# Kernel optimization log

Hardware: AMD Instinct MI355X
Metric: run time of the kernel (lower is better)

The kernel has to match this reference:

```python
import jax, jax.numpy as jnp
import numpy as np

EPS = 1e-8  # torch F.cosine_similarity eps


def setup_inputs() -> dict:
    key = jax.random.key(0)
    k1, k2, k3, k4 = jax.random.split(key, 4)
    B, N, D = 16384, 4096, 1024
    return {
        "query": jax.random.normal(k1, (B, D), dtype=jnp.float32),
        "prompt_components": 0.02 * jax.random.normal(k2, (N, D), dtype=jnp.float32),
        "component_keys": 0.02 * jax.random.normal(k3, (N, D), dtype=jnp.float32),
        "component_attention": 0.02 * jax.random.normal(k4, (N, D), dtype=jnp.float32),
        "top_k": 8,
    }


def reference(query, prompt_components, component_keys, component_attention, top_k):
    # attended query: elementwise scale by mean attention vector
    attn_mean = component_attention.mean(axis=0)            # [D]
    aq = query * attn_mean                                   # [B, D]

    # cosine similarity vs detached keys (vectorized over all components)
    keys = jax.lax.stop_gradient(component_keys)             # detach, as in torch
    aq_n = aq / jnp.maximum(jnp.linalg.norm(aq, axis=1, keepdims=True), EPS)
    k_n = keys / jnp.maximum(jnp.linalg.norm(keys, axis=1, keepdims=True), EPS)
    sims = aq_n @ k_n.T                                      # [B, N]

    top_values, top_indices = jax.lax.top_k(sims, top_k)     # [B, K]
    weights = jax.nn.softmax(top_values, axis=1)             # [B, K]

    # weighted gather-combine of prompt components
    gathered = prompt_components[top_indices]                # [B, K, D]
    selected_prompts = jnp.einsum("bk,bkd->bd", weights, gathered)  # [B, D]
    selected_keys = component_keys[top_indices]              # [B, K, D]

    return selected_prompts[:, None, :], top_indices, selected_keys
```

## Files before the change

### kernel.cpp

```cpp
#include <hip/hip_runtime.h>
#include <math.h>

#define D_DIM 1024
#define N_COMP 4096
#define B_ROWS 16384
#define TOPK 8
#define NC_Q 16
#define NCAND 64
#define EPSV 1e-8f

typedef __bf16 bf16x8 __attribute__((ext_vector_type(8)));
typedef float f32x4 __attribute__((ext_vector_type(4)));

#define WS_MEAN  0
#define WS_KNORM 1024
#define WS_KNN   5120
#define WS_KN16  4199424
#define WS_CI    6296576
#define WS_TW    7345152
#define WS_TI    7476224

__device__ __forceinline__ unsigned short bf16rne(float f) {
    unsigned int u = __float_as_uint(f);
    return (unsigned short)((u + 0x7FFFu + ((u >> 16) & 1u)) >> 16);
}

__device__ __forceinline__ void gload16(const void* g, void* l) {
    __builtin_amdgcn_global_load_lds(
        (const __attribute__((address_space(1))) void*)g,
        (__attribute__((address_space(3))) void*)l, 16, 0, 0);
}

__global__ void seqmean_kernel(const float* __restrict__ attn,
                               float* __restrict__ mean) {
    __shared__ float tile[128][65];
    const int tid = threadIdx.x;
    const int d0 = blockIdx.x * 64;
    const int c = tid & 63, r0 = tid >> 6;
    float acc = 0.f;
    for (int chunk = 0; chunk < 32; ++chunk) {
        const int base = chunk * 128;
        __syncthreads();
        #pragma unroll
        for (int rr = 0; rr < 32; ++rr) {
            int r = r0 * 32 + rr;
            tile[r][c] = attn[(size_t)(base + r) * D_DIM + d0 + c];
        }
        __syncthreads();
        if (tid < 64) {
            #pragma unroll 8
            for (int r = 0; r < 128; ++r)
                acc = __fadd_rn(acc, tile[r][tid]);
        }
    }
    if (tid < 64) mean[d0 + tid] = __fdiv_rn(acc, (float)N_COMP);
}

__global__ void knorm_kernel(const float* __restrict__ keys,
                             float* __restrict__ knorm) {
    const int wave = threadIdx.x >> 6, lane = threadIdx.x & 63;
    const int n = blockIdx.x * 4 + wave;
    const float* x = keys + (size_t)n * D_DIM;
    const int l = lane & 15, g = lane >> 4;
    float lv0, lv1;
    {
        const float* xx = x + g * 128;
        float p[8];
        #pragma unroll
        for (int j = 0; j < 8; ++j) {
            float e = xx[16 * j + l];
            p[j] = __fmul_rn(e, e);
        }
        float t0 = __fadd_rn(p[0], p[1]), t1 = __fadd_rn(p[2], p[3]);
        float t2 = __fadd_rn(p[4], p[5]), t3 = __fadd_rn(p[6], p[7]);
        lv0 = __fadd_rn(__fadd_rn(t0, t1), __fadd_rn(t2, t3));
    }
    {
        const float* xx = x + (g + 4) * 128;
        float p[8];
        #pragma unroll
        for (int j = 0; j < 8; ++j) {
            float e = xx[16 * j + l];
            p[j] = __fmul_rn(e, e);
        }
        float t0 = __fadd_rn(p[0], p[1]), t1 = __fadd_rn(p[2], p[3]);
        float t2 = __fadd_rn(p[4], p[5]), t3 = __fadd_rn(p[6], p[7]);
        lv1 = __fadd_rn(__fadd_rn(t0, t1), __fadd_rn(t2, t3));
    }
    #pragma unroll
    for (int off = 8; off >= 1; off >>= 1) {
        lv0 = __fadd_rn(lv0, __shfl_down(lv0, off));
        lv1 = __fadd_rn(lv1, __shfl_down(lv1, off));
    }
    float L0 = __shfl(lv0, 0),  L1 = __shfl(lv0, 16),
          L2 = __shfl(lv0, 32), L3 = __shfl(lv0, 48);
    float L4 = __shfl(lv1, 0),  L5 = __shfl(lv1, 16),
          L6 = __shfl(lv1, 32), L7 = __shfl(lv1, 48);
    if (lane == 0) {
        float nk = __fadd_rn(
            __fadd_rn(__fadd_rn(L0, L1), __fadd_rn(L2, L3)),
            __fadd_rn(__fadd_rn(L4, L5), __fadd_rn(L6, L7)));
        knorm[n] = fmaxf(__fsqrt_rn(nk), EPSV);
    }
}

__global__ void knn_kernel(const float* __restrict__ keys,
                           const float* __restrict__ knorm,
                           float* __restrict__ knn,
                           unsigned short* __restrict__ kn16) {
    int n = blockIdx.x;
    float kn = knorm[n];
    int d = threadIdx.x * 4;
    const float* row = keys + (size_t)n * D_DIM + d;
    float* orow = knn + (size_t)n * D_DIM + d;
    unsigned short* o16 = kn16 + (size_t)n * D_DIM + d;
    float r0 = __fdiv_rn(row[0], kn);
    float r1 = __fdiv_rn(row[1], kn);
    float r2 = __fdiv_rn(row[2], kn);
    float r3 = __fdiv_rn(row[3], kn);
    orow[0] = r0; orow[1] = r1; orow[2] = r2; orow[3] = r3;
    o16[0] = bf16rne(r0); o16[1] = bf16rne(r1);
    o16[2] = bf16rne(r2); o16[3] = bf16rne(r3);
}

__global__ void aq16_kernel(const float* __restrict__ q,
                            const float* __restrict__ mean,
                            unsigned short* __restrict__ aq16) {
    size_t i = ((size_t)blockIdx.x * 256 + threadIdx.x) * 8;
    int d = (int)(i & (D_DIM - 1));
    float4 a0 = *(const float4*)(q + i);
    float4 a1 = *(const float4*)(q + i + 4);
    float4 m0 = *(const float4*)(mean + d);
    float4 m1 = *(const float4*)(mean + d + 4);
    uint4 pk;
    pk.x = (unsigned)bf16rne(a0.x * m0.x) | ((unsigned)bf16rne(a0.y * m0.y) << 16);
    pk.y = (unsigned)bf16rne(a0.z * m0.z) | ((unsigned)bf16rne(a0.w * m0.w) << 16);
    pk.z = (unsigned)bf16rne(a1.x * m1.x) | ((unsigned)bf16rne(a1.y * m1.y) << 16);
    pk.w = (unsigned)bf16rne(a1.z * m1.z) | ((unsigned)bf16rne(a1.w * m1.w) << 16);
    *(uint4*)(aq16 + i) = pk;
}

__global__ __launch_bounds__(512, 4) void simtop_mfma(
    const unsigned short* __restrict__ aq16,
    const unsigned short* __restrict__ kn16,
    int* __restrict__ candi, float* __restrict__ candv) {
    __shared__ __align__(16) char RAW[49152];
    uint4* A4 = (uint4*)RAW;
    uint4* B4 = (uint4*)(RAW + 16384);
    float* SIM = (float*)RAW;
    float* VM  = (float*)RAW;
    int*   IM  = (int*)(RAW + 16384);

    const int tid = threadIdx.x;
    const int lane = tid & 63;
    const int wid = tid >> 6;
    const int wr = wid >> 2, wc = wid & 3;
    const int l15 = lane & 15, l4 = lane >> 4;
    const int rb = blockIdx.x >> 2;
    const int qq = blockIdx.x & 3;
    const int row0 = rb * 128;
    const int colQ = qq * 1024;
    const int srow = tid & 127;
    const int sstripe = (tid >> 7) & 1;

    float v[NC_Q]; int ix[NC_Q];
    #pragma unroll
    for (int s = 0; s < NC_Q; ++s) { v[s] = -1e30f; ix[s] = 0; }

    for (int ct = 0; ct < 4; ++ct) {
        const int col0 = colQ + ct * 256;
        f32x4 acc[4][4];
        #pragma unroll
        for (int i = 0; i < 4; ++i)
            #pragma unroll
            for (int j = 0; j < 4; ++j) {
                acc[i][j][0] = 0.f; acc[i][j][1] = 0.f;
                acc[i][j][2] = 0.f; acc[i][j][3] = 0.f;
            }

        for (int kt = 0; kt < 16; ++kt) {
            const int k0 = kt * 64;
            __syncthreads();
            #pragma unroll
            for (int c = 0; c < 2; ++c) {
                int unit = c * 512 + tid;
                int r = unit >> 3, j = unit & 7;
                gload16(aq16 + (size_t)(row0 + r) * D_DIM + k0 + (j ^ (r & 7)) * 8,
                        (char*)A4 + unit * 16);
            }
            #pragma unroll
            for (int c = 0; c < 4; ++c) {
                int unit = c * 512 + tid;
                int r = unit >> 3, j = unit & 7;
                gload16(kn16 + (size_t)(col0 + r) * D_DIM + k0 + (j ^ (r & 7)) * 8,
                        (char*)B4 + unit * 16);
            }
            __syncthreads();
            #pragma unroll
            for (int kk = 0; kk < 2; ++kk) {
                bf16x8 af[4], bfv[4];
                #pragma unroll
                for (int f = 0; f < 4; ++f) {
                    int rowa = wr * 64 + f * 16 + l15;
                    int slot = kk * 4 + l4;
                    af[f] = __builtin_bit_cast(bf16x8,
                              A4[rowa * 8 + (slot ^ (rowa & 7))]);
                    int rowb = wc * 64 + f * 16 + l15;
                    bfv[f] = __builtin_bit_cast(bf16x8,
                              B4[rowb * 8 + (slot ^ (rowb & 7))]);
                }
                #pragma unroll
                for (int i = 0; i < 4; ++i)
                    #pragma unroll
                    for (int j = 0; j < 4; ++j)
                        acc[i][j] = __builtin_amdgcn_mfma_f32_16x16x32_bf16(
                            af[i], bfv[j], acc[i][j], 0, 0, 0);
            }
        }
        #pragma unroll 1
        for (int p = 0; p < 4; ++p) {
            __syncthreads();
            if (wr == (p >> 1) && (wc >> 1) == (p & 1)) {
                #pragma unroll
                for (int i = 0; i < 4; ++i)
                    #pragma unroll
                    for (int j = 0; j < 4; ++j)
                        #pragma unroll
                        for (int rg = 0; rg < 4; ++rg)
                            SIM[(i * 16 + l4 * 4 + rg) * 129 +
                                (wc & 1) * 64 + j * 16 + l15] = acc[i][j][rg];
            }
            __syncthreads();
            if (tid < 256 && (srow >> 6) == (p >> 1)) {
                const float* rp = SIM + (srow & 63) * 129 + sstripe * 64;
                const int gbase = col0 + (p & 1) * 128 + sstripe * 64;
                #pragma unroll 1
                for (int cc = 0; cc < 64; ++cc) {
                    float cv = rp[cc];
                    if (cv > v[NC_Q - 1]) {
                        v[NC_Q - 1] = cv; ix[NC_Q - 1] = gbase + cc;
                        #pragma unroll
                        for (int s = NC_Q - 1; s > 0; --s)
                            if (v[s] > v[s - 1]) {
                                float tv = v[s]; v[s] = v[s - 1]; v[s - 1] = tv;
                                int ti = ix[s]; ix[s] = ix[s - 1]; ix[s - 1] = ti;
                            }
                    }
                }
            }
        }
    }
    __syncthreads();
    if (tid < 256) {
        #pragma unroll
        for (int s = 0; s < NC_Q; ++s) {
            VM[tid * 16 + s] = v[s];
            IM[tid * 16 + s] = ix[s];
        }
    }
    __syncthreads();
    if (tid < 128) {
        int ia = 0, ib = 0;
        #pragma unroll 1
        for (int s = 0; s < NC_Q; ++s) {
            float va = (ia < 16) ? VM[tid * 16 + ia] : -3e38f;
            float vb = (ib < 16) ? VM[(tid + 128) * 16 + ib] : -3e38f;
            int id; float vv;
            if (va >= vb) { id = IM[tid * 16 + ia]; vv = va; ++ia; }
            else          { id = IM[(tid + 128) * 16 + ib]; vv = vb; ++ib; }
            candi[(size_t)(row0 + tid) * NCAND + qq * 16 + s] = id;
            candv[(size_t)(row0 + tid) * NCAND + qq * 16 + s] = vv;
        }
    }
}

__global__ __launch_bounds__(256) void rescore_kernel(
    const float* __restrict__ q, const float* __restrict__ knn,
    const float* __restrict__ mean, const int* __restrict__ candi,
    const float* __restrict__ candv,
    float* __restrict__ topw, int* __restrict__ topi) {
    __shared__ float anbuf[D_DIM];
    __shared__ float vbuf[NCAND];
    __shared__ int ibuf[NCAND];
    __shared__ int selid[NCAND];
    __shared__ float snq;
    __shared__ int m_s;
    const int tid = threadIdx.x;
    const int wave = tid >> 6, lane = tid & 63;
    const int b = blockIdx.x;
    const float* qr = q + (size_t)b * D_DIM;

    if (wave == 0) {
        const int l = lane & 15, g = lane >> 4;
        float lv0, lv1;
        {
            const float* x = qr + g * 128;
            const float* m = mean + g * 128;
            float p[8];
            #pragma unroll
            for (int j = 0; j < 8; ++j) {
                float e = __fmul_rn(x[16 * j + l], m[16 * j + l]);
                p[j] = __fmul_rn(e, e);
            }
            float t0 = __fadd_rn(p[0], p[1]), t1 = __fadd_rn(p[2], p[3]);
            float t2 = __fadd_rn(p[4], p[5]), t3 = __fadd_rn(p[6], p[7]);
            lv0 = __fadd_rn(__fadd_rn(t0, t1), __fadd_rn(t2, t3));
        }
        {
            const float* x = qr + (g + 4) * 128;
            const float* m = mean + (g + 4) * 128;
            float p[8];
            #pragma unroll
            for (int j = 0; j < 8; ++j) {
                float e = __fmul_rn(x[16 * j + l], m[16 * j + l]);
                p[j] = __fmul_rn(e, e);
            }
            float t0 = __fadd_rn(p[0], p[1]), t1 = __fadd_rn(p[2], p[3]);
            float t2 = __fadd_rn(p[4], p[5]), t3 = __fadd_rn(p[6], p[7]);
            lv1 = __fadd_rn(__fadd_rn(t0, t1), __fadd_rn(t2, t3));
        }
        #pragma unroll
        for (int off = 8; off >= 1; off >>= 1) {
            lv0 = __fadd_rn(lv0, __shfl_down(lv0, off));
            lv1 = __fadd_rn(lv1, __shfl_down(lv1, off));
        }
        float L0 = __shfl(lv0, 0),  L1 = __shfl(lv0, 16),
              L2 = __shfl(lv0, 32), L3 = __shfl(lv0, 48);
        float L4 = __shfl(lv1, 0),  L5 = __shfl(lv1, 16),
              L6 = __shfl(lv1, 32), L7 = __shfl(lv1, 48);
        if (lane == 0) {
            float nq = __fadd_rn(
                __fadd_rn(__fadd_rn(L0, L1), __fadd_rn(L2, L3)),
                __fadd_rn(__fadd_rn(L4, L5), __fadd_rn(L6, L7)));
            snq = fmaxf(__fsqrt_rn(nq), EPSV);
        }
    }
    __syncthreads();
    const float nqd = snq;

    {
        int d0 = tid * 4;
        float4 qv = *(const float4*)(qr + d0);
        float4 mv = *(const float4*)(mean + d0);
        anbuf[d0 + 0] = __fdiv_rn(__fmul_rn(qv.x, mv.x), nqd);
        anbuf[d0 + 1] = __fdiv_rn(__fmul_rn(qv.y, mv.y), nqd);
        anbuf[d0 + 2] = __fdiv_rn(__fmul_rn(qv.z, mv.z), nqd);
        anbuf[d0 + 3] = __fdiv_rn(__fmul_rn(qv.w, mv.w), nqd);
    }

    if (wave == 1) {
        float av = candv[(size_t)b * NCAND + lane];
        int aid = candi[(size_t)b * NCAND + lane];
        float t8;
        {
            float vv = av; int vid = aid;
            #pragma unroll
            for (int s = 0; s < TOPK; ++s) {
                float bv = vv; int bid = vid;
                #pragma unroll
                for (int off = 32; off >= 1; off >>= 1) {
                    float ov = __shfl_xor(bv, off);
                    int oid = __shfl_xor(bid, off);
                    if (ov > bv || (ov == bv && oid < bid)) { bv = ov; bid = oid; }
                }
                t8 = bv;
                if (vid == bid) vv = -1e30f;
            }
        }
        float thr = t8 - 0.003f * nqd;
        bool sel = (av >= thr);
        unsigned long long mk = __ballot(sel);
        int pos = __popcll(mk & ((1ull << lane) - 1ull));
        if (sel) selid[pos] = aid;
        if (lane == 0) m_s = (int)__popcll(mk);
    }
    __syncthreads();
    const int m = m_s;

    {
        const int s = tid >> 2, chunk = tid & 3;
        if (s < m) {
            const int id = selid[s];
            const int start = chunk * 320;
            const int n4 = (chunk == 3) ? 16 : 80;
            const float4* k4 = (const float4*)(knn + (size_t)id * D_DIM + start);
            const float4* a4 = (const float4*)(anbuf + start);
            float acc = 0.f;
            #pragma unroll 4
            for (int t = 0; t < n4; ++t) {
                float4 kv = k4[t];
                float4 av4 = a4[t];
                acc = __fmaf_rn(av4.x, kv.x, acc);
                acc = __fmaf_rn(av4.y, kv.y, acc);
                acc = __fmaf_rn(av4.z, kv.z, acc);
                acc = __fmaf_rn(av4.w, kv.w, acc);
            }
            float c2 = __shfl_down(acc, 1);
            float c3 = __shfl_down(acc, 2);
            float c4 = __shfl_down(acc, 3);
            if (chunk == 0) {
                vbuf[s] = __fadd_rn(__fadd_rn(__fadd_rn(acc, c2), c3), c4);
                ibuf[s] = id;
            }
        }
    }
    __syncthreads();

    if (wave == 0) {
        float v = (lane < m) ? vbuf[lane] : -3e38f;
        int id = (lane < m) ? ibuf[lane] : 0x7fffffff;
        float sv[TOPK]; int si[TOPK];
        #pragma unroll
        for (int s = 0; s < TOPK; ++s) {
            float bv = v; int bid = id;
            #pragma unroll
            for (int off = 32; off >= 1; off >>= 1) {
                float ov = __shfl_xor(bv, off);
                int oid = __shfl_xor(bid, off);
                if (ov > bv || (ov == bv && oid < bid)) { bv = ov; bid = oid; }
            }
            sv[s] = bv; si[s] = bid;
            if (id == bid) v = -3e38f;
        }
        if (lane == 0) {
            float mx = sv[0];
            float w[TOPK];
            float ssum = 0.f;
            #pragma unroll
            for (int k = 0; k < TOPK; ++k) { w[k] = expf(sv[k] - mx); ssum += w[k]; }
            float rs = 1.0f / ssum;
            #pragma unroll
            for (int k = 0; k < TOPK; ++k) {
                topw[b * TOPK + k] = w[k] * rs;
                topi[b * TOPK + k] = si[k];
            }
        }
    }
}

__global__ void output_kernel(const float* __restrict__ topw,
                              const int* __restrict__ topi,
                              const float* __restrict__ prompts,
                              const float* __restrict__ keys,
                              float* __restrict__ out) {
    int b = blockIdx.x;
    float w[TOPK];
    int id[TOPK];
    #pragma unroll
    for (int k = 0; k < TOPK; ++k) {
        w[k] = topw[b * TOPK + k];
        id[k] = topi[b * TOPK + k];
    }

    const size_t OFF1 = (size_t)B_ROWS * D_DIM;
    const size_t OFF2 = OFF1 + (size_t)B_ROWS * TOPK;

    if (threadIdx.x < TOPK)
        out[OFF1 + (size_t)b * TOPK + threadIdx.x] = (float)id[threadIdx.x];

    int d0 = threadIdx.x * 4;
    float4 acc; acc.x = acc.y = acc.z = acc.w = 0.f;
    #pragma unroll
    for (int k = 0; k < TOPK; ++k) {
        const float* pr = prompts + (size_t)id[k] * D_DIM + d0;
        float4 pv = *(const float4*)pr;
        acc.x += w[k] * pv.x; acc.y += w[k] * pv.y;
        acc.z += w[k] * pv.z; acc.w += w[k] * pv.w;
        const float* kr = keys + (size_t)id[k] * D_DIM + d0;
        float4 kv = *(const float4*)kr;
        *(float4*)(out + OFF2 + ((size_t)b * TOPK + k) * D_DIM + d0) = kv;
    }
    *(float4*)(out + (size_t)b * D_DIM + d0) = acc;
}

extern "C" void kernel_launch(void* const* d_in, const int* in_sizes, int n_in,
                              void* d_out, int out_size, void* d_ws, size_t ws_size,
                              hipStream_t stream) {
    const float* query   = (const float*)d_in[0];
    const float* prompts = (const float*)d_in[1];
    const float* keys    = (const float*)d_in[2];
    const float* attn    = (const float*)d_in[3];
    float* ws = (float*)d_ws;
    float* out = (float*)d_out;

    float* mean  = ws + WS_MEAN;
    float* knorm = ws + WS_KNORM;
    float* knn   = ws + WS_KNN;
    unsigned short* kn16 = (unsigned short*)(ws + WS_KN16);
    int*   candi = (int*)(ws + WS_CI);
    float* topw  = ws + WS_TW;
    int*   topi  = (int*)(ws + WS_TI);
    float* outscratch = out + (size_t)B_ROWS * D_DIM + (size_t)B_ROWS * TOPK;
    unsigned short* aq16 = (unsigned short*)outscratch;
    float* candv = outscratch + 8388608;

    seqmean_kernel<<<16, 256, 0, stream>>>(attn, mean);
    knorm_kernel<<<N_COMP / 4, 256, 0, stream>>>(keys, knorm);
    knn_kernel<<<N_COMP, 256, 0, stream>>>(keys, knorm, knn, kn16);
    aq16_kernel<<<8192, 256, 0, stream>>>(query, mean, aq16);
    simtop_mfma<<<512, 512, 0, stream>>>(aq16, kn16, candi, candv);
    rescore_kernel<<<B_ROWS, 256, 0, stream>>>(query, knn, mean, candi, candv,
                                               topw, topi);
    output_kernel<<<B_ROWS, 256, 0, stream>>>(topw, topi, prompts, keys, out);
}
```

Baseline: 951.7 us.

## Double-buffer LDS tiles in similarity GEMM and shrink column tile to 128

Restructures the MFMA similarity/top-k kernel into a flat 128-step loop over 128-column tiles with double-buffered LDS staging, so the next tile's global-to-LDS loads are issued before computing the current one, synchronised with vmcnt waits and raw barriers. Accumulators shrink from 4x4 to 4x2 fragments and the SIM scratch uses a 68-wide padded layout, processed in two passes per column tile. This is meant to hide global load latency and reduce register pressure, at the cost of 64KB LDS per block, which can lower occupancy, and more frequent top-k insertion phases that still serialise on half the threads.

```diff
diff --git a/kernel.cpp b/kernel.cpp
--- a/kernel.cpp
+++ b/kernel.cpp
@@ -30,6 +30,9 @@
         (const __attribute__((address_space(1))) void*)g,
         (__attribute__((address_space(3))) void*)l, 16, 0, 0);
 }
+
+#define RAW_BARRIER() do { asm volatile("" ::: "memory"); \
+    __builtin_amdgcn_s_barrier(); asm volatile("" ::: "memory"); } while (0)
 
 __global__ void seqmean_kernel(const float* __restrict__ attn,
                                float* __restrict__ mean) {
@@ -140,15 +143,15 @@
     *(uint4*)(aq16 + i) = pk;
 }
 
+#define SIMW 68
+#define NSTEP 128
 __global__ __launch_bounds__(512, 4) void simtop_mfma(
     const unsigned short* __restrict__ aq16,
     const unsigned short* __restrict__ kn16,
     int* __restrict__ candi, float* __restrict__ candv) {
-    __shared__ __align__(16) char RAW[49152];
-    uint4* A4 = (uint4*)RAW;
-    uint4* B4 = (uint4*)(RAW + 16384);
+    __shared__ __align__(16) char RAW[65536];
     float* SIM = (float*)RAW;
-    float* VM  = (float*)RAW;
+    float* MV  = (float*)RAW;
     int*   IM  = (int*)(RAW + 16384);
 
     const int tid = threadIdx.x;
@@ -167,109 +170,141 @@
     #pragma unroll
     for (int s = 0; s < NC_Q; ++s) { v[s] = -1e30f; ix[s] = 0; }
 
-    for (int ct = 0; ct < 4; ++ct) {
-        const int col0 = colQ + ct * 256;
-        f32x4 acc[4][4];
-        #pragma unroll
-        for (int i = 0; i < 4; ++i)
-            #pragma unroll
-            for (int j = 0; j < 4; ++j) {
-                acc[i][j][0] = 0.f; acc[i][j][1] = 0.f;
-                acc[i][j][2] = 0.f; acc[i][j][3] = 0.f;
-            }
-
-        for (int kt = 0; kt < 16; ++kt) {
-            const int k0 = kt * 64;
+    f32x4 acc[4][2];
+    #pragma unroll
+    for (int i = 0; i < 4; ++i)
+        #pragma unroll
+        for (int j = 0; j < 2; ++j) {
+            acc[i][j][0] = 0.f; acc[i][j][1] = 0.f;
+            acc[i][j][2] = 0.f; acc[i][j][3] = 0.f;
+        }
+
+    auto stage = [&](int t) {
+        char* base = RAW + (t & 1) * 32768;
+        const int k0 = (t & 15) * 64;
+        const int col0 = colQ + (t >> 4) * 128;
+        #pragma unroll
+        for (int c = 0; c < 2; ++c) {
+            int unit = c * 512 + tid;
+            int r = unit >> 3, j = unit & 7;
+            gload16(aq16 + (size_t)(row0 + r) * D_DIM + k0 + (j ^ (r & 7)) * 8,
+                    base + unit * 16);
+        }
+        #pragma unroll
+        for (int c = 0; c < 2; ++c) {
+            int unit = c * 512 + tid;
+            int r = unit >> 3, j = unit & 7;
+            gload16(kn16 + (size_t)(col0 + r) * D_DIM + k0 + (j ^ (r & 7)) * 8,
+                    base + 16384 + unit * 16);
+        }
+    };
+
+    stage(0);
+    for (int t = 0; t < NSTEP; ++t) {
+        const bool ctend = ((t & 15) == 15);
+        if (!ctend) {
+            stage(t + 1);
+            asm volatile("s_waitcnt vmcnt(4)" ::: "memory");
+        } else {
+            asm volatile("s_waitcnt vmcnt(0)" ::: "memory");
+        }
+        RAW_BARRIER();
+
+        const uint4* A4 = (const uint4*)(RAW + (t & 1) * 32768);
+        const uint4* B4 = (const uint4*)(RAW + (t & 1) * 32768 + 16384);
+        #pragma unroll
+        for (int kk = 0; kk < 2; ++kk) {
+            bf16x8 af[4], bfv[2];
+            #pragma unroll
+            for (int f = 0; f < 4; ++f) {
+                int rowa = wr * 64 + f * 16 + l15;
+                int slot = kk * 4 + l4;
+                af[f] = __builtin_bit_cast(bf16x8,
+                          A4[rowa * 8 + (slot ^ (rowa & 7))]);
+            }
+            #pragma unroll
+            for (int j = 0; j < 2; ++j) {
+                int rowb = wc * 32 + j * 16 + l15;
+                int slot = kk * 4 + l4;
+                bfv[j] = __builtin_bit_cast(bf16x8,
+                          B4[rowb * 8 + (slot ^ (rowb & 7))]);
+            }
+            #pragma unroll
+            for (int i = 0; i < 4; ++i)
+                #pragma unroll
+                for (int j = 0; j < 2; ++j)
+                    acc[i][j] = __builtin_amdgcn_mfma_f32_16x16x32_bf16(
+                        af[i], bfv[j], acc[i][j], 0, 0, 0);
+        }
+
+        if (!ctend) {
+            RAW_BARRIER();
+        } else {
             __syncthreads();
-            #pragma unroll
-            for (int c = 0; c < 2; ++c) {
-                int unit = c * 512 + tid;
-                int r = unit >> 3, j = unit & 7;
-                gload16(aq16 + (size_t)(row0 + r) * D_DIM + k0 + (j ^ (r & 7)) * 8,
-                        (char*)A4 + unit * 16);
-            }
-            #pragma unroll
-            for (int c = 0; c < 4; ++c) {
-                int unit = c * 512 + tid;
-                int r = unit >> 3, j = unit & 7;
-                gload16(kn16 + (size_t)(col0 + r) * D_DIM + k0 + (j ^ (r & 7)) * 8,
-                        (char*)B4 + unit * 16);
-            }
-            __syncthreads();
-            #pragma unroll
-            for (int kk = 0; kk < 2; ++kk) {
-                bf16x8 af[4], bfv[4];
-                #pragma unroll
-                for (int f = 0; f < 4; ++f) {
-                    int rowa = wr * 64 + f * 16 + l15;
-                    int slot = kk * 4 + l4;
-                    af[f] = __builtin_bit_cast(bf16x8,
-                              A4[rowa * 8 + (slot ^ (rowa & 7))]);
-                    int rowb = wc * 64 + f * 16 + l15;
-                    bfv[f] = __builtin_bit_cast(bf16x8,
-                              B4[rowb * 8 + (slot ^ (rowb & 7))]);
+            const int col0 = colQ + (t >> 4) * 128;
+            #pragma unroll 1
+            for (int p = 0; p < 2; ++p) {
+                if ((wc >> 1) == p) {
+                    #pragma unroll
+                    for (int i = 0; i < 4; ++i)
+                        #pragma unroll
+                        for (int j = 0; j < 2; ++j)
+                            #pragma unroll
+                            for (int rg = 0; rg < 4; ++rg)
+                                SIM[(wr * 64 + i * 16 + l4 * 4 + rg) * SIMW +
+                                    (wc & 1) * 32 + j * 16 + l15] = acc[i][j][rg];
                 }
-                #pragma unroll
-                for (int i = 0; i < 4; ++i)
-                    #pragma unroll
-                    for (int j = 0; j < 4; ++j)
-                        acc[i][j] = __builtin_amdgcn_mfma_f32_16x16x32_bf16(
-                            af[i], bfv[j], acc[i][j], 0, 0, 0);
-            }
-        }
-        #pragma unroll 1
-        for (int p = 0; p < 4; ++p) {
-            __syncthreads();
-            if (wr == (p >> 1) && (wc >> 1) == (p & 1)) {
-                #pragma unroll
-                for (int i = 0; i < 4; ++i)
-                    #pragma unroll
-                    for (int j = 0; j < 4; ++j)
-                        #pragma unroll
-                        for (int rg = 0; rg < 4; ++rg)
-                            SIM[(i * 16 + l4 * 4 + rg) * 129 +
-                                (wc & 1) * 64 + j * 16 + l15] = acc[i][j][rg];
-            }
-            __syncthreads();
-            if (tid < 256 && (srow >> 6) == (p >> 1)) {
-                const float* rp = SIM + (srow & 63) * 129 + sstripe * 64;
-                const int gbase = col0 + (p & 1) * 128 + sstripe * 64;
-                #pragma unroll 1
-                for (int cc = 0; cc < 64; ++cc) {
-                    float cv = rp[cc];
-                    if (cv > v[NC_Q - 1]) {
-                        v[NC_Q - 1] = cv; ix[NC_Q - 1] = gbase + cc;
-                        #pragma unroll
-                        for (int s = NC_Q - 1; s > 0; --s)
-                            if (v[s] > v[s - 1]) {
-                                float tv = v[s]; v[s] = v[s - 1]; v[s - 1] = tv;
-                                int ti = ix[s]; ix[s] = ix[s - 1]; ix[s - 1] = ti;
-                            }
+                __syncthreads();
+                if (tid < 256) {
+                    const float* rp = SIM + srow * SIMW + sstripe * 32;
+                    const int gbase = col0 + p * 64 + sstripe * 32;
+                    #pragma unroll 1
+                    for (int c = 0; c < 32; ++c) {
+                        float cv = rp[c];
+                        if (cv > v[NC_Q - 1]) {
+                            v[NC_Q - 1] = cv; ix[NC_Q - 1] = gbase + c;
+                            #pragma unroll
+                            for (int s = NC_Q - 1; s > 0; --s)
+                                if (v[s] > v[s - 1]) {
+                                    float tv = v[s]; v[s] = v[s - 1]; v[s - 1] = tv;
+                                    int ti = ix[s]; ix[s] = ix[s - 1]; ix[s - 1] = ti;
+                                }
+                        }
                     }
                 }
-            }
+                __syncthreads();
+            }
+            #pragma unroll
+            for (int i = 0; i < 4; ++i)
+                #pragma unroll
+                for (int j = 0; j < 2; ++j) {
+                    acc[i][j][0] = 0.f; acc[i][j][1] = 0.f;
+                    acc[i][j][2] = 0.f; acc[i][j][3] = 0.f;
+                }
+            if (t < NSTEP - 1) stage(t + 1);
         }
     }
     __syncthreads();
     if (tid < 256) {
         #pragma unroll
         for (int s = 0; s < NC_Q; ++s) {
-            VM[tid * 16 + s] = v[s];
+            MV[tid * 16 + s] = v[s];
             IM[tid * 16 + s] = ix[s];
         }
     }
     __syncthreads();
     if (tid < 128) {
         int ia = 0, ib = 0;
+        size_t obase = (size_t)(row0 + tid) * NCAND + qq * 16;
         #pragma unroll 1
         for (int s = 0; s < NC_Q; ++s) {
-            float va = (ia < 16) ? VM[tid * 16 + ia] : -3e38f;
-            float vb = (ib < 16) ? VM[(tid + 128) * 16 + ib] : -3e38f;
+            float va = (ia < 16) ? MV[tid * 16 + ia] : -3e38f;
+            float vb = (ib < 16) ? MV[(tid + 128) * 16 + ib] : -3e38f;
             int id; float vv;
             if (va >= vb) { id = IM[tid * 16 + ia]; vv = va; ++ia; }
             else          { id = IM[(tid + 128) * 16 + ib]; vv = vb; ++ib; }
-            candi[(size_t)(row0 + tid) * NCAND + qq * 16 + s] = id;
-            candv[(size_t)(row0 + tid) * NCAND + qq * 16 + s] = vv;
+            candi[obase + s] = id;
+            candv[obase + s] = vv;
         }
     }
 }
```

Measured after the change: 1.030 ms. 8.2% more time.
